# Performance work log

Measured on AMD Instinct MI355X. Metric: run time of the kernel, lower is better.

The kernel has to match this reference:

```python
import jax, jax.numpy as jnp
import numpy as np

N_NODES = 100000


def _sage_conv(x, src, dst, w_l, b_l, w_r):
    # PyG SAGEConv (aggr='mean', root_weight=True):
    #   out = lin_l(mean_{j in N(i)} x_j) + lin_r(x_i)
    # messages flow src (row 0) -> dst (row 1)
    msgs = x[src]                                             # [E, d]
    agg = jax.ops.segment_sum(msgs, dst, num_segments=N_NODES)  # [N, d]
    cnt = jax.ops.segment_sum(jnp.ones((src.shape[0], 1), x.dtype), dst,
                              num_segments=N_NODES)           # [N, 1]
    mean = agg / jnp.maximum(cnt, 1.0)
    return mean @ w_l + b_l + x @ w_r


def setup_inputs() -> dict:
    key = jax.random.key(0)
    ks = jax.random.split(key, 8)
    in_dim, hid, out = 128, 64, 128
    n_edges = 1600000
    x = jax.random.normal(ks[0], (N_NODES, in_dim), dtype=jnp.float32)
    edge_index = jax.random.randint(ks[1], (2, n_edges), 0, N_NODES, dtype=jnp.int64)
    s1 = 1.0 / np.sqrt(in_dim)
    s2 = 1.0 / np.sqrt(hid)
    return {
        "x": x,
        "edge_index": edge_index,
        "w1_l": jax.random.uniform(ks[2], (in_dim, hid), jnp.float32, -s1, s1),
        "b1": jnp.zeros((hid,), jnp.float32),
        "w1_r": jax.random.uniform(ks[3], (in_dim, hid), jnp.float32, -s1, s1),
        "w2_l": jax.random.uniform(ks[4], (hid, out), jnp.float32, -s2, s2),
        "b2": jnp.zeros((out,), jnp.float32),
        "w2_r": jax.random.uniform(ks[5], (hid, out), jnp.float32, -s2, s2),
    }


def reference(x, edge_index, w1_l, b1, w1_r, w2_l, b2, w2_r):
    src, dst = edge_index[0], edge_index[1]
    h = jax.nn.relu(_sage_conv(x, src, dst, w1_l, b1, w1_r))
    h = _sage_conv(h, src, dst, w2_l, b2, w2_r)
    return h
```

## Files before the change

kernel.cpp:

```cpp
#include <hip/hip_runtime.h>

#define N_NODES 100000
#define NBUCK   782
#define NBUCK2  784
#define NGRP    8
#define P1TILE  4096
#define SLAB    4096
#define SUBSLAB 512
#define AGG_CAP 512

typedef __bf16 bf16x8 __attribute__((ext_vector_type(8)));
typedef float floatx4 __attribute__((ext_vector_type(4)));
typedef float floatx2 __attribute__((ext_vector_type(2)));

static __device__ __forceinline__ unsigned short f2bf(float f) {
  unsigned u = __float_as_uint(f);
  u += 0x7fff + ((u >> 16) & 1);
  return (unsigned short)(u >> 16);
}

__global__ __launch_bounds__(256) void init_kernel(
    int* __restrict__ bucket_cursor,
    const float* __restrict__ w1_l, const float* __restrict__ w1_r,
    const float* __restrict__ w2_l, const float* __restrict__ w2_r,
    unsigned short* __restrict__ Wt1, unsigned short* __restrict__ Wt2) {
  int gid = blockIdx.x * 256 + threadIdx.x;
  if (gid < NGRP * NBUCK2 + 2) bucket_cursor[gid] = 0;
  int n = gid >> 7, k = gid & 127;
  float v1 = (n < 64) ? w1_l[k * 64 + n] : w1_r[k * 64 + (n - 64)];
  Wt1[n * 128 + k] = f2bf(v1);
  float v2 = (k < 64) ? w2_l[k * 128 + n] : w2_r[(k - 64) * 128 + n];
  Wt2[n * 128 + k] = f2bf(v2);
}

__global__ __launch_bounds__(512) void part_gemm1_kernel(
    const int* __restrict__ src, const int* __restrict__ dst,
    int* __restrict__ bucket_cursor, unsigned* __restrict__ pairs,
    int n_edges, int nb_part,
    const float* __restrict__ x, const unsigned short* __restrict__ Wt1,
    const float* __restrict__ b1, unsigned short* __restrict__ ZB1, int M) {
  __shared__ __align__(16) char smem[44224];
  int t = threadIdx.x;

  if ((int)blockIdx.x >= nb_part) {
    unsigned short* As = (unsigned short*)smem;
    int node0 = ((int)blockIdx.x - nb_part) * 128;
    #pragma unroll
    for (int i = 0; i < 8; ++i) {
      int c = t + i * 512;
      int row = c >> 5, c4 = (c & 31) * 4;
      float4 v = make_float4(0.f, 0.f, 0.f, 0.f);
      if (node0 + row < M) v = *(const float4*)&x[(long)(node0 + row) * 128 + c4];
      ushort4 o;
      o.x = f2bf(v.x); o.y = f2bf(v.y); o.z = f2bf(v.z); o.w = f2bf(v.w);
      *(ushort4*)&As[row * 136 + c4] = o;
    }
    __syncthreads();
    int w8 = t >> 6, lane = t & 63;
    int m = lane & 15, q = lane >> 4;
    int w = w8 & 3, half = w8 >> 2;
    int col0 = w * 32, rowbase = half * 64;
    floatx4 acc[4][2];
    #pragma unroll
    for (int rt = 0; rt < 4; ++rt)
      #pragma unroll
      for (int ct = 0; ct < 2; ++ct) acc[rt][ct] = (floatx4){0.f, 0.f, 0.f, 0.f};
    #pragma unroll
    for (int ks = 0; ks < 4; ++ks) {
      bf16x8 b0 = *(const bf16x8*)&Wt1[(col0 + m) * 128 + ks * 32 + q * 8];
      bf16x8 bb = *(const bf16x8*)&Wt1[(col0 + 16 + m) * 128 + ks * 32 + q * 8];
      #pragma unroll
      for (int rt = 0; rt < 4; ++rt) {
        bf16x8 a = *(const bf16x8*)&As[(rowbase + rt * 16 + m) * 136 + ks * 32 + q * 8];
        acc[rt][0] = __builtin_amdgcn_mfma_f32_16x16x32_bf16(a, b0, acc[rt][0], 0, 0, 0);
        acc[rt][1] = __builtin_amdgcn_mfma_f32_16x16x32_bf16(a, bb, acc[rt][1], 0, 0, 0);
      }
    }
    #pragma unroll
    for (int ct = 0; ct < 2; ++ct) {
      int col = col0 + ct * 16 + m;
      float bv = (col >= 64) ? b1[col - 64] : 0.f;
      #pragma unroll
      for (int rt = 0; rt < 4; ++rt) {
        #pragma unroll
        for (int i = 0; i < 4; ++i) {
          int row = node0 + rowbase + rt * 16 + q * 4 + i;
          if (row >= M) continue;
          ZB1[(long)row * 128 + col] = f2bf(acc[rt][ct][i] + bv);
        }
      }
    }
    return;
  }

  int2* sorted = (int2*)smem;
  int* hist  = (int*)(smem + 32768);
  int* scan_ = hist + NBUCK;
  int* gbase = scan_ + NBUCK;
  int* tmp   = gbase + NBUCK;
  int g = (int)blockIdx.x & (NGRP - 1);
  long e0 = (long)blockIdx.x * P1TILE;
  int n = (int)min((long)P1TILE, (long)n_edges - e0);

  for (int b = t; b < NBUCK; b += 512) hist[b] = 0;
  __syncthreads();
  for (int i = t; i < n; i += 512) atomicAdd(&hist[dst[e0 + i] >> 7], 1);
  __syncthreads();

  int loc[2];
  int s = 0;
  #pragma unroll
  for (int j = 0; j < 2; ++j) {
    int idx = 2 * t + j;
    loc[j] = s;
    s += (idx < NBUCK) ? hist[idx] : 0;
  }
  tmp[t] = s;
  __syncthreads();
  for (int off = 1; off < 512; off <<= 1) {
    int u = (t >= off) ? tmp[t - off] : 0;
    __syncthreads();
    tmp[t] += u;
    __syncthreads();
  }
  int excl = tmp[t] - s;
  #pragma unroll
  for (int j = 0; j < 2; ++j) {
    int idx = 2 * t + j;
    if (idx < NBUCK) scan_[idx] = excl + loc[j];
  }
  __syncthreads();

  for (int b = t; b < NBUCK; b += 512) {
    int c = hist[b];
    gbase[b] = c ? atomicAdd(&bucket_cursor[g * NBUCK2 + b], c) : 0;
    hist[b] = scan_[b];
  }
  __syncthreads();

  for (int i = t; i < n; i += 512) {
    int sv = src[e0 + i];
    int dv = dst[e0 + i];
    int r = atomicAdd(&hist[dv >> 7], 1);
    sorted[r] = make_int2(sv, dv);
  }
  __syncthreads();

  for (int i = t; i < n; i += 512) {
    int2 p = sorted[i];
    int b = p.y >> 7;
    int pos = gbase[b] + (i - scan_[b]);
    if (pos < SUBSLAB) {
      unsigned pk = (unsigned)p.x | ((unsigned)(p.y & 127) << 17);
      pairs[(long)b * SLAB + (g << 9) + pos] = pk;
    }
  }
}

__global__ __launch_bounds__(512) void bucket_csr_kernel(
    const unsigned* __restrict__ pairs, const int* __restrict__ bucket_cnt,
    int2* __restrict__ offsets2, int* __restrict__ src_sorted, int n_nodes) {
  __shared__ unsigned sp[SLAB];
  __shared__ int lout[SLAB];
  __shared__ int ndeg[128];
  __shared__ int nsc[128];
  __shared__ int cnt8[NGRP];
  __shared__ int pref8[NGRP + 1];
  int b = blockIdx.x;
  int node0 = b << 7;
  int t = threadIdx.x;
  long sbeg = (long)b * SLAB;
  if (t < NGRP) cnt8[t] = min(bucket_cnt[t * NBUCK2 + b], SUBSLAB);
  if (t < 128) ndeg[t] = 0;
  __syncthreads();
  if (t == 0) {
    int s = 0;
    #pragma unroll
    for (int gi = 0; gi < NGRP; ++gi) { pref8[gi] = s; s += cnt8[gi]; }
    pref8[NGRP] = s;
  }
  __syncthreads();
  int m = pref8[NGRP];

  for (int gi = 0; gi < NGRP; ++gi) {
    int c = cnt8[gi], p0 = pref8[gi];
    for (int i = t; i < c; i += 512) {
      unsigned p = pairs[sbeg + (gi << 9) + i];
      sp[p0 + i] = p;
      atomicAdd(&ndeg[p >> 17], 1);
    }
  }
  __syncthreads();

  if (t < 128) nsc[t] = ndeg[t];
  __syncthreads();
  for (int off = 1; off < 128; off <<= 1) {
    int u = 0;
    if (t < 128 && t >= off) u = nsc[t - off];
    __syncthreads();
    if (t < 128) nsc[t] += u;
    __syncthreads();
  }
  if (t < 128) {
    int excl = nsc[t] - ndeg[t];
    int node = node0 + t;
    if (node < n_nodes)
      offsets2[node] = make_int2((int)sbeg + excl, (int)sbeg + nsc[t]);
    ndeg[t] = excl;
  }
  __syncthreads();

  for (int i = t; i < m; i += 512) {
    unsigned p = sp[i];
    int r = atomicAdd(&ndeg[p >> 17], 1);
    lout[r] = (int)(p & 0x1FFFFu);
  }
  __syncthreads();
  for (int i = t; i < m; i += 512) src_sorted[sbeg + i] = lout[i];
}

__global__ __launch_bounds__(256) void mfma_gemm2_kernel(
    const unsigned short* __restrict__ A, const unsigned short* __restrict__ Wt,
    const float* __restrict__ bias, float* __restrict__ Y, int M) {
  __shared__ unsigned short As[64 * 136];
  int node0 = blockIdx.x * 64;
  int t = threadIdx.x;
  #pragma unroll
  for (int i = 0; i < 4; ++i) {
    int c = t + i * 256;
    int row = c >> 4, c8 = (c & 15) * 8;
    uint4 v = make_uint4(0u, 0u, 0u, 0u);
    if (node0 + row < M) v = *(const uint4*)&A[(long)(node0 + row) * 128 + c8];
    *(uint4*)&As[row * 136 + c8] = v;
  }
  __syncthreads();
  int w = t >> 6, lane = t & 63;
  int m = lane & 15, q = lane >> 4;
  int col0 = w * 32;
  floatx4 acc[4][2];
  #pragma unroll
  for (int rt = 0; rt < 4; ++rt)
    #pragma unroll
    for (int ct = 0; ct < 2; ++ct) acc[rt][ct] = (floatx4){0.f, 0.f, 0.f, 0.f};

  #pragma unroll
  for (int ks = 0; ks < 4; ++ks) {
    bf16x8 b0 = *(const bf16x8*)&Wt[(col0 + m) * 128 + ks * 32 + q * 8];
    bf16x8 b1 = *(const bf16x8*)&Wt[(col0 + 16 + m) * 128 + ks * 32 + q * 8];
    #pragma unroll
    for (int rt = 0; rt < 4; ++rt) {
      bf16x8 a = *(const bf16x8*)&As[(rt * 16 + m) * 136 + ks * 32 + q * 8];
      acc[rt][0] = __builtin_amdgcn_mfma_f32_16x16x32_bf16(a, b0, acc[rt][0], 0, 0, 0);
      acc[rt][1] = __builtin_amdgcn_mfma_f32_16x16x32_bf16(a, b1, acc[rt][1], 0, 0, 0);
    }
  }
  #pragma unroll
  for (int ct = 0; ct < 2; ++ct) {
    int col = col0 + ct * 16 + m;
    float bv = bias[col];
    #pragma unroll
    for (int rt = 0; rt < 4; ++rt) {
      #pragma unroll
      for (int i = 0; i < 4; ++i) {
        int row = node0 + rt * 16 + q * 4 + i;
        if (row >= M) continue;
        Y[(long)row * 128 + col] = acc[rt][ct][i] + bv;
      }
    }
  }
}

#define ACC_P(A, v)                                                            \
  do {                                                                         \
    A[0] += (floatx2){__uint_as_float((v).x << 16),                            \
                      __uint_as_float((v).x & 0xffff0000u)};                   \
    A[1] += (floatx2){__uint_as_float((v).y << 16),                            \
                      __uint_as_float((v).y & 0xffff0000u)};                   \
    A[2] += (floatx2){__uint_as_float((v).z << 16),                            \
                      __uint_as_float((v).z & 0xffff0000u)};                   \
    A[3] += (floatx2){__uint_as_float((v).w << 16),                            \
                      __uint_as_float((v).w & 0xffff0000u)};                   \
  } while (0)

template <bool FUSE_RELU>
__global__ __launch_bounds__(256) void aggregate_bf16_kernel(
    const unsigned short* __restrict__ gsrc, const unsigned short* __restrict__ zadd,
    unsigned short* __restrict__ outp, const int2* __restrict__ offsets2,
    const int* __restrict__ src_sorted, int n_nodes) {
  __shared__ int stage[4 * AGG_CAP];
  int wv = threadIdx.x >> 6;
  int lane = threadIdx.x & 63;
  int wid = (blockIdx.x << 2) | wv;
  int node8 = wid << 3;
  int sub = lane >> 3;
  int sl  = lane & 7;
  int node = node8 + sub;
  bool wvalid = (node8 < n_nodes);
  bool nvalid = wvalid && (node < n_nodes);

  int wbeg = 0, wend = 0, beg = 0, end = 0;
  if (wvalid) {
    wbeg = offsets2[node8].x;
    wend = offsets2[min(node8 + 8, n_nodes) - 1].y;
  }
  if (nvalid) {
    int2 o = offsets2[node];
    beg = o.x; end = o.y;
  }
  int deg = end - beg;
  int cnt = wend - wbeg;
  int* my = &stage[wv * AGG_CAP];
  bool staged = wvalid && (cnt <= AGG_CAP);
  if (staged) {
    for (int i = lane; i < cnt; i += 64) my[i] = src_sorted[wbeg + i];
  }
  __syncthreads();

  const unsigned short* base = gsrc + sl * 8;
  floatx2 A0[4], A1[4], A2[4], A3[4];
  #pragma unroll
  for (int i = 0; i < 4; ++i) {
    A0[i] = (floatx2){0.f, 0.f}; A1[i] = (floatx2){0.f, 0.f};
    A2[i] = (floatx2){0.f, 0.f}; A3[i] = (floatx2){0.f, 0.f};
  }

  if (staged) {
    int lb = beg - wbeg;
    int e = 0;
    for (; e + 8 <= deg; e += 8) {
      int s0 = my[lb + e];
      int s1 = my[lb + e + 1];
      int s2 = my[lb + e + 2];
      int s3 = my[lb + e + 3];
      int s4 = my[lb + e + 4];
      int s5 = my[lb + e + 5];
      int s6 = my[lb + e + 6];
      int s7 = my[lb + e + 7];
      uint4 v0 = *(const uint4*)(base + (long)s0 * 128);
      uint4 v1 = *(const uint4*)(base + (long)s1 * 128);
      uint4 v2 = *(const uint4*)(base + (long)s2 * 128);
      uint4 v3 = *(const uint4*)(base + (long)s3 * 128);
      uint4 v4 = *(const uint4*)(base + (long)s4 * 128);
      uint4 v5 = *(const uint4*)(base + (long)s5 * 128);
      uint4 v6 = *(const uint4*)(base + (long)s6 * 128);
      uint4 v7 = *(const uint4*)(base + (long)s7 * 128);
      ACC_P(A0, v0); ACC_P(A1, v1); ACC_P(A2, v2); ACC_P(A3, v3);
      ACC_P(A0, v4); ACC_P(A1, v5); ACC_P(A2, v6); ACC_P(A3, v7);
    }
    if (e + 4 <= deg) {
      int s0 = my[lb + e];
      int s1 = my[lb + e + 1];
      int s2 = my[lb + e + 2];
      int s3 = my[lb + e + 3];
      uint4 v0 = *(const uint4*)(base + (long)s0 * 128);
      uint4 v1 = *(const uint4*)(base + (long)s1 * 128);
      uint4 v2 = *(const uint4*)(base + (long)s2 * 128);
      uint4 v3 = *(const uint4*)(base + (long)s3 * 128);
      ACC_P(A0, v0); ACC_P(A1, v1); ACC_P(A2, v2); ACC_P(A3, v3);
      e += 4;
    }
    for (; e < deg; ++e) {
      int s0 = my[lb + e];
      uint4 v0 = *(const uint4*)(base + (long)s0 * 128);
      ACC_P(A0, v0);
    }
  } else if (nvalid) {
    for (int e = beg; e < end; ++e) {
      int s0 = src_sorted[e];
      uint4 v0 = *(const uint4*)(base + (long)s0 * 128);
      ACC_P(A0, v0);
    }
  }
  #pragma unroll
  for (int i = 0; i < 4; ++i) A0[i] = (A0[i] + A1[i]) + (A2[i] + A3[i]);

  if (nvalid) {
    float inv = 1.f / fmaxf((float)deg, 1.f);
    float r[8];
    r[0] = A0[0].x * inv; r[1] = A0[0].y * inv;
    r[2] = A0[1].x * inv; r[3] = A0[1].y * inv;
    r[4] = A0[2].x * inv; r[5] = A0[2].y * inv;
    r[6] = A0[3].x * inv; r[7] = A0[3].y * inv;
    if (FUSE_RELU) {
      uint4 z = *(const uint4*)&zadd[(long)node * 128 + sl * 8];
      r[0] = fmaxf(r[0] + __uint_as_float(z.x << 16), 0.f);
      r[1] = fmaxf(r[1] + __uint_as_float(z.x & 0xffff0000u), 0.f);
      r[2] = fmaxf(r[2] + __uint_as_float(z.y << 16), 0.f);
      r[3] = fmaxf(r[3] + __uint_as_float(z.y & 0xffff0000u), 0.f);
      r[4] = fmaxf(r[4] + __uint_as_float(z.z << 16), 0.f);
      r[5] = fmaxf(r[5] + __uint_as_float(z.z & 0xffff0000u), 0.f);
      r[6] = fmaxf(r[6] + __uint_as_float(z.w << 16), 0.f);
      r[7] = fmaxf(r[7] + __uint_as_float(z.w & 0xffff0000u), 0.f);
    }
    uint4 ov;
    ov.x = (unsigned)f2bf(r[0]) | ((unsigned)f2bf(r[1]) << 16);
    ov.y = (unsigned)f2bf(r[2]) | ((unsigned)f2bf(r[3]) << 16);
    ov.z = (unsigned)f2bf(r[4]) | ((unsigned)f2bf(r[5]) << 16);
    ov.w = (unsigned)f2bf(r[6]) | ((unsigned)f2bf(r[7]) << 16);
    *(uint4*)&outp[(long)node * 128 + sl * 8] = ov;
  }
}
#undef ACC_P

extern "C" void kernel_launch(void* const* d_in, const int* in_sizes, int n_in,
                              void* d_out, int out_size, void* d_ws, size_t ws_size,
                              hipStream_t stream) {
  const float* x    = (const float*)d_in[0];
  const int*   ei   = (const int*)d_in[1];
  const float* w1_l = (const float*)d_in[2];
  const float* b1   = (const float*)d_in[3];
  const float* w1_r = (const float*)d_in[4];
  const float* w2_l = (const float*)d_in[5];
  const float* b2   = (const float*)d_in[6];
  const float* w2_r = (const float*)d_in[7];
  float* out = (float*)d_out;

  const int E = in_sizes[1] / 2;
  const int* src = ei;
  const int* dst = ei + E;

  unsigned short* ZB1 = (unsigned short*)d_ws;
  unsigned short* ZB2 = ZB1 + (long)N_NODES * 128;
  unsigned short* Wt1 = ZB2 + (long)N_NODES * 128;
  unsigned short* Wt2 = Wt1 + 16384;
  int* bucket_cursor = (int*)(Wt2 + 16384);
  int2* offsets2     = (int2*)(bucket_cursor + NGRP * NBUCK2 + 2);
  int* src_sorted    = (int*)(offsets2 + N_NODES);
  unsigned* pairs    = (unsigned*)(src_sorted + (long)NBUCK * SLAB);

  int nb_part = (E + P1TILE - 1) / P1TILE;
  int gemm1_blocks = (N_NODES + 127) / 128;

  init_kernel<<<64, 256, 0, stream>>>(bucket_cursor, w1_l, w1_r, w2_l, w2_r,
                                      Wt1, Wt2);
  part_gemm1_kernel<<<nb_part + gemm1_blocks, 512, 0, stream>>>(
      src, dst, bucket_cursor, pairs, E, nb_part, x, Wt1, b1, ZB1, N_NODES);
  bucket_csr_kernel<<<NBUCK, 512, 0, stream>>>(pairs, bucket_cursor,
                                               offsets2, src_sorted, N_NODES);

  int agg_blocks = (N_NODES + 31) / 32;
  aggregate_bf16_kernel<true><<<agg_blocks, 256, 0, stream>>>(
      ZB1, ZB1 + 64, ZB2 + 64, offsets2, src_sorted, N_NODES);
  aggregate_bf16_kernel<false><<<agg_blocks, 256, 0, stream>>>(
      ZB2 + 64, nullptr, ZB2, offsets2, src_sorted, N_NODES);
  mfma_gemm2_kernel<<<(N_NODES + 63) / 64, 256, 0, stream>>>(
      ZB2, Wt2, b2, out, N_NODES);
}
```

Measured before the change: 230.9 us.

## Split fused partition+GEMM1 kernel into separate partition and GEMM1 kernels

```diff
diff --git a/kernel.cpp b/kernel.cpp
--- a/kernel.cpp
+++ b/kernel.cpp
@@ -33,71 +33,16 @@
   Wt2[n * 128 + k] = f2bf(v2);
 }
 
-__global__ __launch_bounds__(512) void part_gemm1_kernel(
+__global__ __launch_bounds__(512) void bucket_partition_kernel(
     const int* __restrict__ src, const int* __restrict__ dst,
     int* __restrict__ bucket_cursor, unsigned* __restrict__ pairs,
-    int n_edges, int nb_part,
-    const float* __restrict__ x, const unsigned short* __restrict__ Wt1,
-    const float* __restrict__ b1, unsigned short* __restrict__ ZB1, int M) {
-  __shared__ __align__(16) char smem[44224];
+    int n_edges) {
+  __shared__ int2 sorted[P1TILE];
+  __shared__ int hist[NBUCK];
+  __shared__ int scan_[NBUCK];
+  __shared__ int gbase[NBUCK];
+  __shared__ int tmp[512];
   int t = threadIdx.x;
-
-  if ((int)blockIdx.x >= nb_part) {
-    unsigned short* As = (unsigned short*)smem;
-    int node0 = ((int)blockIdx.x - nb_part) * 128;
-    #pragma unroll
-    for (int i = 0; i < 8; ++i) {
-      int c = t + i * 512;
-      int row = c >> 5, c4 = (c & 31) * 4;
-      float4 v = make_float4(0.f, 0.f, 0.f, 0.f);
-      if (node0 + row < M) v = *(const float4*)&x[(long)(node0 + row) * 128 + c4];
-      ushort4 o;
-      o.x = f2bf(v.x); o.y = f2bf(v.y); o.z = f2bf(v.z); o.w = f2bf(v.w);
-      *(ushort4*)&As[row * 136 + c4] = o;
-    }
-    __syncthreads();
-    int w8 = t >> 6, lane = t & 63;
-    int m = lane & 15, q = lane >> 4;
-    int w = w8 & 3, half = w8 >> 2;
-    int col0 = w * 32, rowbase = half * 64;
-    floatx4 acc[4][2];
-    #pragma unroll
-    for (int rt = 0; rt < 4; ++rt)
-      #pragma unroll
-      for (int ct = 0; ct < 2; ++ct) acc[rt][ct] = (floatx4){0.f, 0.f, 0.f, 0.f};
-    #pragma unroll
-    for (int ks = 0; ks < 4; ++ks) {
-      bf16x8 b0 = *(const bf16x8*)&Wt1[(col0 + m) * 128 + ks * 32 + q * 8];
-      bf16x8 bb = *(const bf16x8*)&Wt1[(col0 + 16 + m) * 128 + ks * 32 + q * 8];
-      #pragma unroll
-      for (int rt = 0; rt < 4; ++rt) {
-        bf16x8 a = *(const bf16x8*)&As[(rowbase + rt * 16 + m) * 136 + ks * 32 + q * 8];
-        acc[rt][0] = __builtin_amdgcn_mfma_f32_16x16x32_bf16(a, b0, acc[rt][0], 0, 0, 0);
-        acc[rt][1] = __builtin_amdgcn_mfma_f32_16x16x32_bf16(a, bb, acc[rt][1], 0, 0, 0);
-      }
-    }
-    #pragma unroll
-    for (int ct = 0; ct < 2; ++ct) {
-      int col = col0 + ct * 16 + m;
-      float bv = (col >= 64) ? b1[col - 64] : 0.f;
-      #pragma unroll
-      for (int rt = 0; rt < 4; ++rt) {
-        #pragma unroll
-        for (int i = 0; i < 4; ++i) {
-          int row = node0 + rowbase + rt * 16 + q * 4 + i;
-          if (row >= M) continue;
-          ZB1[(long)row * 128 + col] = f2bf(acc[rt][ct][i] + bv);
-        }
-      }
-    }
-    return;
-  }
-
-  int2* sorted = (int2*)smem;
-  int* hist  = (int*)(smem + 32768);
-  int* scan_ = hist + NBUCK;
-  int* gbase = scan_ + NBUCK;
-  int* tmp   = gbase + NBUCK;
   int g = (int)blockIdx.x & (NGRP - 1);
   long e0 = (long)blockIdx.x * P1TILE;
   int n = (int)min((long)P1TILE, (long)n_edges - e0);
@@ -217,6 +162,59 @@
   }
   __syncthreads();
   for (int i = t; i < m; i += 512) src_sorted[sbeg + i] = lout[i];
+}
+
+__global__ __launch_bounds__(256) void mfma_gemm1_kernel(
+    const float* __restrict__ A, const unsigned short* __restrict__ Wt,
+    const float* __restrict__ bias, unsigned short* __restrict__ Y, int M) {
+  __shared__ unsigned short As[64 * 136];
+  int node0 = blockIdx.x * 64;
+  int t = threadIdx.x;
+  #pragma unroll
+  for (int i = 0; i < 8; ++i) {
+    int c = t + i * 256;
+    int row = c >> 5, c4 = (c & 31) * 4;
+    float4 v = make_float4(0.f, 0.f, 0.f, 0.f);
+    if (node0 + row < M) v = *(const float4*)&A[(long)(node0 + row) * 128 + c4];
+    ushort4 o;
+    o.x = f2bf(v.x); o.y = f2bf(v.y); o.z = f2bf(v.z); o.w = f2bf(v.w);
+    *(ushort4*)&As[row * 136 + c4] = o;
+  }
+  __syncthreads();
+  int w = t >> 6, lane = t & 63;
+  int m = lane & 15, q = lane >> 4;
+  int col0 = w * 32;
+  floatx4 acc[4][2];
+  #pragma unroll
+  for (int rt = 0; rt < 4; ++rt)
+    #pragma unroll
+    for (int ct = 0; ct < 2; ++ct) acc[rt][ct] = (floatx4){0.f, 0.f, 0.f, 0.f};
+
+  #pragma unroll
+  for (int ks = 0; ks < 4; ++ks) {
+    bf16x8 b0 = *(const bf16x8*)&Wt[(col0 + m) * 128 + ks * 32 + q * 8];
+    bf16x8 b1 = *(const bf16x8*)&Wt[(col0 + 16 + m) * 128 + ks * 32 + q * 8];
+    #pragma unroll
+    for (int rt = 0; rt < 4; ++rt) {
+      bf16x8 a = *(const bf16x8*)&As[(rt * 16 + m) * 136 + ks * 32 + q * 8];
+      acc[rt][0] = __builtin_amdgcn_mfma_f32_16x16x32_bf16(a, b0, acc[rt][0], 0, 0, 0);
+      acc[rt][1] = __builtin_amdgcn_mfma_f32_16x16x32_bf16(a, b1, acc[rt][1], 0, 0, 0);
+    }
+  }
+  #pragma unroll
+  for (int ct = 0; ct < 2; ++ct) {
+    int col = col0 + ct * 16 + m;
+    float bv = (col >= 64) ? bias[col - 64] : 0.f;
+    #pragma unroll
+    for (int rt = 0; rt < 4; ++rt) {
+      #pragma unroll
+      for (int i = 0; i < 4; ++i) {
+        int row = node0 + rt * 16 + q * 4 + i;
+        if (row >= M) continue;
+        Y[(long)row * 128 + col] = f2bf(acc[rt][ct][i] + bv);
+      }
+    }
+  }
 }
 
 __global__ __launch_bounds__(256) void mfma_gemm2_kernel(
@@ -429,20 +427,21 @@
   unsigned* pairs    = (unsigned*)(src_sorted + (long)NBUCK * SLAB);
 
   int nb_part = (E + P1TILE - 1) / P1TILE;
-  int gemm1_blocks = (N_NODES + 127) / 128;
+  int gemm_blocks = (N_NODES + 63) / 64;
 
   init_kernel<<<64, 256, 0, stream>>>(bucket_cursor, w1_l, w1_r, w2_l, w2_r,
                                       Wt1, Wt2);
-  part_gemm1_kernel<<<nb_part + gemm1_blocks, 512, 0, stream>>>(
-      src, dst, bucket_cursor, pairs, E, nb_part, x, Wt1, b1, ZB1, N_NODES);
+  bucket_partition_kernel<<<nb_part, 512, 0, stream>>>(
+      src, dst, bucket_cursor, pairs, E);
   bucket_csr_kernel<<<NBUCK, 512, 0, stream>>>(pairs, bucket_cursor,
                                                offsets2, src_sorted, N_NODES);
+  mfma_gemm1_kernel<<<gemm_blocks, 256, 0, stream>>>(x, Wt1, b1, ZB1, N_NODES);
 
   int agg_blocks = (N_NODES + 31) / 32;
   aggregate_bf16_kernel<true><<<agg_blocks, 256, 0, stream>>>(
       ZB1, ZB1 + 64, ZB2 + 64, offsets2, src_sorted, N_NODES);
   aggregate_bf16_kernel<false><<<agg_blocks, 256, 0, stream>>>(
       ZB2 + 64, nullptr, ZB2, offsets2, src_sorted, N_NODES);
-  mfma_gemm2_kernel<<<(N_NODES + 63) / 64, 256, 0, stream>>>(
+  mfma_gemm2_kernel<<<gemm_blocks, 256, 0, stream>>>(
       ZB2, Wt2, b2, out, N_NODES);
 }
```

Result: slower. 240.7 us (+4.2%).
